# Performance work log

Measured on AMD Instinct MI355X. Metric: run time of the kernel, lower is better.

The kernel has to match this reference:

```python
import jax, jax.numpy as jnp
import numpy as np
from jax import lax

PATCH = 11          # patch_size
DIL = 2             # dilation_patch
PAD = (PATCH // 2) * DIL  # 10
EPS = 1e-5


def setup_inputs() -> dict:
    key = jax.random.key(0)
    k0, k1, kw, kb, kg, kbe = jax.random.split(key, 6)
    B, C, H, W = 8, 128, 192, 192
    x0 = jax.random.normal(k0, (B, C, H, W), dtype=jnp.float32)
    x1 = jax.random.normal(k1, (B, C, H, W), dtype=jnp.float32)
    # Conv2d(121, 8, k=3, s=1, p=1) params + BatchNorm2d(8) affine params
    conv_w = jax.random.normal(kw, (8, 121, 3, 3), dtype=jnp.float32) * 0.05
    conv_b = jax.random.normal(kb, (8,), dtype=jnp.float32) * 0.05
    gamma = jnp.ones((8,), dtype=jnp.float32)
    beta = jnp.zeros((8,), dtype=jnp.float32)
    return {"x0": x0, "x1": x1, "conv_w": conv_w, "conv_b": conv_b,
            "gamma": gamma, "beta": beta}


def _correlation(x0, x1):
    """spatial_correlation_sample(kernel=1, patch=11, stride=1, pad=0, dil_patch=2).
    out[b, pi*11+pj, i, j] = sum_c x0[b,c,i,j] * x1[b,c, i+(pi-5)*2, j+(pj-5)*2]
    (zero-padded outside)."""
    x1p = jnp.pad(x1, ((0, 0), (0, 0), (PAD, PAD), (PAD, PAD)))
    slices = []
    for pi in range(PATCH):       # static 11x11 displacement grid
        for pj in range(PATCH):
            x1s = lax.dynamic_slice(x1p, (0, 0, pi * DIL, pj * DIL), x1.shape)
            slices.append(jnp.einsum('bchw,bchw->bhw', x0, x1s))
    return jnp.stack(slices, axis=1)  # [B, 121, H, W]


def reference(x0, x1, conv_w, conv_b, gamma, beta):
    y = _correlation(x0, x1)  # [B, 121, H, W]
    y = lax.conv_general_dilated(y, conv_w, window_strides=(1, 1),
                                 padding=((1, 1), (1, 1)),
                                 dimension_numbers=('NCHW', 'OIHW', 'NCHW'))
    y = y + conv_b[None, :, None, None]
    # BatchNorm2d in training mode: batch statistics over (B, H, W), biased var
    mean = jnp.mean(y, axis=(0, 2, 3))
    var = jnp.var(y, axis=(0, 2, 3))
    y = (y - mean[None, :, None, None]) * (gamma / jnp.sqrt(var + EPS))[None, :, None, None] \
        + beta[None, :, None, None]
    return jax.nn.relu(y)
```

## Files before the change

kernel.cpp:

```cpp
#include <hip/hip_runtime.h>

#define HH 192
#define WW 192
#define CC 128
#define BB 8
#define HW (HH * WW)
#define OC 8
#define NPIX (BB * HW)
#define YCHUNK (OC * BB * HW)
#define X0ROW 24576
#define X1ROW 28672

typedef __attribute__((ext_vector_type(8))) short bf16x8;
typedef __attribute__((ext_vector_type(4))) float f32x4;

__device__ __forceinline__ unsigned short f2bf(float f) {
    unsigned int u = __float_as_uint(f);
    u += 0x7fffu + ((u >> 16) & 1u);
    return (unsigned short)(u >> 16);
}

__global__ __launch_bounds__(256) void k_pack(
    const float* __restrict__ x0, const float* __restrict__ x1,
    unsigned short* __restrict__ x0t, unsigned short* __restrict__ x1t)
{
    const int h = blockIdx.x, b = blockIdx.y, t = blockIdx.z;
    const float* src = t ? x1 : x0;
    __shared__ unsigned short lds[WW * 130];

    for (int idx = threadIdx.x; idx < CC * WW; idx += 256) {
        const int w = idx % WW, c = idx / WW;
        lds[w * 130 + c] = f2bf(src[((size_t)(b * CC + c) * HH + h) * WW + w]);
    }
    __syncthreads();

    if (t == 0) {
        unsigned int* dst = (unsigned int*)(x0t + (size_t)(b * HH + h) * X0ROW);
        for (int f2 = threadIdx.x; f2 < X0ROW / 2; f2 += 256) {
            const int e2  = f2 & 3;
            const int pxl = (f2 >> 2) & 15;
            const int kg  = (f2 >> 6) & 3;
            const int q   = (f2 >> 8) & 3;
            const int pu  = f2 >> 10;
            const int ut  = pu % 6, par = pu / 6;
            const int px  = 2 * (16 * ut + pxl) + par;
            const int c   = q * 32 + kg * 8 + e2 * 2;
            const unsigned int lo = lds[px * 130 + c];
            const unsigned int hi = lds[px * 130 + c + 1];
            dst[f2] = lo | (hi << 16);
        }
    } else {
        unsigned int* dst = (unsigned int*)(x1t + (size_t)(b * HH + h) * X1ROW);
        for (int f2 = threadIdx.x; f2 < X1ROW / 2; f2 += 256) {
            const int e2  = f2 & 3;
            const int pxl = (f2 >> 2) & 15;
            const int kg  = (f2 >> 6) & 3;
            const int q   = (f2 >> 8) & 3;
            const int pv  = f2 >> 10;
            const int vt  = pv % 7, par = pv / 7;
            const int v   = 16 * vt - 8 + pxl;
            unsigned int val = 0;
            if (v >= 0 && v < 96) {
                const int px = 2 * v + par;
                const int c  = q * 32 + kg * 8 + e2 * 2;
                val = lds[px * 130 + c] | ((unsigned int)lds[px * 130 + c + 1] << 16);
            }
            dst[f2] = val;
        }
    }
}

__global__ __launch_bounds__(384, 3) void k_corr_mfma_conv(
    const unsigned short* __restrict__ x0t, const unsigned short* __restrict__ x1t,
    const float* __restrict__ cw, const float* __restrict__ cb,
    float* __restrict__ y0, float* __restrict__ y1)
{
    const int L = blockIdx.x;
    const int w = (L & 7) * 64 + (L >> 3);
    const int b     = w >> 6;
    const int rem   = w & 63;
    const int part  = rem >> 5;
    const int strip = rem & 31;
    const int i0    = strip * 6;
    const int plo   = part ? 6 : 0;
    const int phi   = part ? 11 : 6;

    const int tid  = threadIdx.x;
    const int wave = tid >> 6, lane = tid & 63;
    const int ln15 = lane & 15, kg = lane >> 4;
    const int u0   = wave * 16;

    __shared__ float corr[8][194][11];

    if (tid < 176) {
        const int ir = tid / 22, rr = tid % 22;
        const int pj = rr % 11, jj = (rr < 11) ? 0 : 193;
        corr[ir][jj][pj] = 0.f;
    }

    float yacc[3][OC];
#pragma unroll
    for (int k = 0; k < 3; ++k)
#pragma unroll
        for (int o = 0; o < OC; ++o) yacc[k][o] = 0.f;

    const int jt  = tid % 192;
    const int irb = tid / 192;

    const unsigned short* x0b = x0t + (size_t)b * HH * X0ROW;
    const unsigned short* x1b = x1t + (size_t)b * HH * X1ROW;

    for (int pi = plo; pi < phi; ++pi) {
        __syncthreads();

        for (int ir = 0; ir < 8; ++ir) {
            const int i = i0 - 1 + ir;
            const int r = i + 2 * pi - 10;
            const bool gv = (i >= 0) && (i < HH) && (r >= 0) && (r < HH);
            const int icl = min(max(i, 0), HH - 1);
            const int rcl = min(max(r, 0), HH - 1);
            const unsigned short* arow = x0b + (size_t)icl * X0ROW + lane * 8;
            const unsigned short* brow = x1b + (size_t)rcl * X1ROW + lane * 8;

#pragma unroll
            for (int par = 0; par < 2; ++par) {
                const unsigned short* pa = arow + (par * 6 + wave) * 2048;
                const bf16x8 a0 = *(const bf16x8*)(pa);
                const bf16x8 a1 = *(const bf16x8*)(pa + 512);
                const bf16x8 a2 = *(const bf16x8*)(pa + 1024);
                const bf16x8 a3 = *(const bf16x8*)(pa + 1536);

#pragma unroll
                for (int vtl = 0; vtl < 2; ++vtl) {
                    const unsigned short* pb =
                        brow + (par * 7 + wave + vtl) * 2048;
                    const bf16x8 b0 = *(const bf16x8*)(pb);
                    const bf16x8 b1 = *(const bf16x8*)(pb + 512);
                    const bf16x8 b2 = *(const bf16x8*)(pb + 1024);
                    const bf16x8 b3 = *(const bf16x8*)(pb + 1536);

                    f32x4 c = {0.f, 0.f, 0.f, 0.f};
                    c = __builtin_amdgcn_mfma_f32_16x16x32_bf16(a0, b0, c, 0, 0, 0);
                    c = __builtin_amdgcn_mfma_f32_16x16x32_bf16(a1, b1, c, 0, 0, 0);
                    c = __builtin_amdgcn_mfma_f32_16x16x32_bf16(a2, b2, c, 0, 0, 0);
                    c = __builtin_amdgcn_mfma_f32_16x16x32_bf16(a3, b3, c, 0, 0, 0);

                    const int v = u0 - 8 + 16 * vtl + ln15;
#pragma unroll
                    for (int rg = 0; rg < 4; ++rg) {
                        const int u  = u0 + kg * 4 + rg;
                        const int pj = v - u + 5;
                        if (pj >= 0 && pj < 11)
                            corr[ir][2 * u + par + 1][pj] = gv ? c[rg] : 0.f;
                    }
                }
            }
        }
        __syncthreads();

        for (int ki = 0; ki < 3; ++ki) {
            for (int kj = 0; kj < 3; ++kj) {
                float cv[3][11];
#pragma unroll
                for (int k = 0; k < 3; ++k) {
                    const float* cp = &corr[irb + 2 * k + ki][jt + kj][0];
#pragma unroll
                    for (int pj = 0; pj < 11; ++pj) cv[k][pj] = cp[pj];
                }
#pragma unroll
                for (int o = 0; o < OC; ++o) {
                    float a0 = yacc[0][o], a1 = yacc[1][o], a2 = yacc[2][o];
#pragma unroll
                    for (int pj = 0; pj < 11; ++pj) {
                        const float wv =
                            cw[o * 1089 + (pi * 11 + pj) * 9 + ki * 3 + kj];
                        a0 = fmaf(wv, cv[0][pj], a0);
                        a1 = fmaf(wv, cv[1][pj], a1);
                        a2 = fmaf(wv, cv[2][pj], a2);
                    }
                    yacc[0][o] = a0; yacc[1][o] = a1; yacc[2][o] = a2;
                }
            }
        }
    }

    float* yp = part ? y1 : y0;
#pragma unroll
    for (int k = 0; k < 3; ++k) {
        const int irow = i0 + irb + 2 * k;
#pragma unroll
        for (int o = 0; o < OC; ++o) {
            float val = yacc[k][o];
            if (part == 0) val += cb[o];
            yp[((size_t)(b * OC + o) * HH + irow) * WW + jt] = val;
        }
    }
}

__global__ __launch_bounds__(256) void k_corr_conv(
    const float* __restrict__ x0, const float* __restrict__ x1,
    const float* __restrict__ cw, const float* __restrict__ cb,
    float* __restrict__ y)
{
    const int b  = blockIdx.z;
    const int i0 = blockIdx.y * 14;
    const int j0 = blockIdx.x * 14;
    const int li = threadIdx.x >> 4;
    const int lj = threadIdx.x & 15;
    const int gi = i0 + li - 1;
    const int gj = j0 + lj - 1;
    const bool valid    = (gi >= 0) & (gi < HH) & (gj >= 0) & (gj < WW);
    const bool interior = (li >= 1) & (li <= 14) & (lj >= 1) & (lj <= 14)
                        & (gi < HH) & (gj < WW);

    __shared__ float corr[16][16][13];

    float yacc[OC];
#pragma unroll
    for (int o = 0; o < OC; ++o) yacc[o] = 0.f;

    const size_t bbase = (size_t)b * CC * HW;
    const float* x0p = x0 + bbase + (size_t)gi * WW + gj;

    for (int pi = 0; pi < 11; ++pi) {
        float acc[11];
#pragma unroll
        for (int k = 0; k < 11; ++k) acc[k] = 0.f;

        const int r = gi + 2 * pi - 10;
        if (valid && r >= 0 && r < HH) {
            const float* p0 = x0p;
            if (gj >= 10 && gj <= WW - 11) {
                const float* p1o = x1 + bbase + (size_t)r * WW + (gj - 10);
#pragma unroll 2
                for (int c = 0; c < CC; ++c) {
                    const float a = *p0;
#pragma unroll
                    for (int k = 0; k < 11; ++k)
                        acc[k] = fmaf(a, p1o[2 * k], acc[k]);
                    p0 += HW; p1o += HW;
                }
            } else {
                const float* p1 = x1 + bbase + (size_t)r * WW;
#pragma unroll 2
                for (int c = 0; c < CC; ++c) {
                    const float a = *p0;
#pragma unroll
                    for (int k = 0; k < 11; ++k) {
                        const int col = gj + 2 * k - 10;
                        const float v = (col >= 0 && col < WW) ? p1[col] : 0.f;
                        acc[k] = fmaf(a, v, acc[k]);
                    }
                    p0 += HW; p1 += HW;
                }
            }
        }

        __syncthreads();
#pragma unroll
        for (int k = 0; k < 11; ++k) corr[li][lj][k] = acc[k];
        __syncthreads();

        if (interior) {
#pragma unroll
            for (int ki = 0; ki < 3; ++ki) {
#pragma unroll
                for (int kj = 0; kj < 3; ++kj) {
                    float cv[11];
#pragma unroll
                    for (int k = 0; k < 11; ++k)
                        cv[k] = corr[li + ki - 1][lj + kj - 1][k];
#pragma unroll
                    for (int o = 0; o < OC; ++o) {
#pragma unroll
                        for (int k = 0; k < 11; ++k) {
                            const float wv =
                                cw[(((o * 121) + pi * 11 + k) * 3 + ki) * 3 + kj];
                            yacc[o] = fmaf(wv, cv[k], yacc[o]);
                        }
                    }
                }
            }
        }
    }

    if (interior) {
#pragma unroll
        for (int o = 0; o < OC; ++o)
            y[(size_t)(b * OC + o) * HW + (size_t)gi * WW + gj] = yacc[o] + cb[o];
    }
}

__global__ __launch_bounds__(256) void k_stats_partial(
    const float* __restrict__ y0, const float* __restrict__ y1, int add2,
    float* __restrict__ st)
{
    const int bid = blockIdx.x;
    const int b = bid >> 5, rem = bid & 31;
    const int o = rem >> 2, q = rem & 3;
    const size_t off = (size_t)(b * OC + o) * (HW / 4) + q * (HW / 16);
    const float4* p0 = (const float4*)y0 + off;
    const float4* p1 = (const float4*)y1 + off;
    float s = 0.f, qq = 0.f;
    for (int t = threadIdx.x; t < HW / 16; t += 256) {
        float4 z = p0[t];
        if (add2) {
            const float4 v = p1[t];
            z.x += v.x; z.y += v.y; z.z += v.z; z.w += v.w;
        }
        s += z.x + z.y + z.z + z.w;
        qq = fmaf(z.x, z.x, qq); qq = fmaf(z.y, z.y, qq);
        qq = fmaf(z.z, z.z, qq); qq = fmaf(z.w, z.w, qq);
    }
#pragma unroll
    for (int off2 = 32; off2 > 0; off2 >>= 1) {
        s  += __shfl_down(s, off2);
        qq += __shfl_down(qq, off2);
    }
    __shared__ float ss[4], sq[4];
    const int lane = threadIdx.x & 63, wv = threadIdx.x >> 6;
    if (lane == 0) { ss[wv] = s; sq[wv] = qq; }
    __syncthreads();
    if (threadIdx.x == 0) {
        st[bid]       = ss[0] + ss[1] + ss[2] + ss[3];
        st[256 + bid] = sq[0] + sq[1] + sq[2] + sq[3];
    }
}

__global__ void k_stats_final(float* __restrict__ st,
                              const float* __restrict__ gamma,
                              const float* __restrict__ beta)
{
    const int o = threadIdx.x;
    if (o < 8) {
        float S = 0.f, Q = 0.f;
#pragma unroll
        for (int b = 0; b < 8; ++b)
#pragma unroll
            for (int q = 0; q < 4; ++q) {
                S += st[b * 32 + o * 4 + q];
                Q += st[256 + b * 32 + o * 4 + q];
            }
        const float invN = 1.f / (float)NPIX;
        const float mean = S * invN;
        const float var  = Q * invN - mean * mean;
        const float sc   = gamma[o] / sqrtf(var + 1e-5f);
        st[512 + o] = sc;
        st[520 + o] = beta[o] - mean * sc;
    }
}

__global__ __launch_bounds__(256) void k_bn_relu(
    const float* __restrict__ y0, const float* __restrict__ y1, int add2,
    const float* __restrict__ st, float* __restrict__ out)
{
    const int i = blockIdx.x * 256 + threadIdx.x;
    const int o = (i / (HW / 4)) & 7;
    const float sc = st[512 + o], sh = st[520 + o];
    float4 z = ((const float4*)y0)[i];
    if (add2) {
        const float4 v = ((const float4*)y1)[i];
        z.x += v.x; z.y += v.y; z.z += v.z; z.w += v.w;
    }
    float4 r;
    r.x = fmaxf(fmaf(z.x, sc, sh), 0.f);
    r.y = fmaxf(fmaf(z.y, sc, sh), 0.f);
    r.z = fmaxf(fmaf(z.z, sc, sh), 0.f);
    r.w = fmaxf(fmaf(z.w, sc, sh), 0.f);
    ((float4*)out)[i] = r;
}

extern "C" void kernel_launch(void* const* d_in, const int* in_sizes, int n_in,
                              void* d_out, int out_size, void* d_ws, size_t ws_size,
                              hipStream_t stream)
{
    const float* x0    = (const float*)d_in[0];
    const float* x1    = (const float*)d_in[1];
    const float* cw    = (const float*)d_in[2];
    const float* cb    = (const float*)d_in[3];
    const float* gamma = (const float*)d_in[4];
    const float* beta  = (const float*)d_in[5];
    float* out = (float*)d_out;
    float* st  = (float*)d_ws;

    const size_t x0bytes = (size_t)BB * HH * X0ROW * sizeof(unsigned short);
    const size_t x1bytes = (size_t)BB * HH * X1ROW * sizeof(unsigned short);
    const size_t ybytes  = (size_t)YCHUNK * sizeof(float);

    if (ws_size >= x0bytes + x1bytes + ybytes) {
        unsigned short* x0t = (unsigned short*)d_ws;
        unsigned short* x1t = (unsigned short*)((char*)d_ws + x0bytes);
        float* y1           = (float*)((char*)d_ws + x0bytes + x1bytes);

        k_pack<<<dim3(HH, BB, 2), 256, 0, stream>>>(x0, x1, x0t, x1t);
        k_corr_mfma_conv<<<512, 384, 0, stream>>>(x0t, x1t, cw, cb, out, y1);
        k_stats_partial<<<256, 256, 0, stream>>>(out, y1, 1, st);
        k_stats_final<<<1, 64, 0, stream>>>(st, gamma, beta);
        k_bn_relu<<<(YCHUNK / 4) / 256, 256, 0, stream>>>(out, y1, 1, st, out);
    } else {
        dim3 g1(14, 14, 8);
        k_corr_conv<<<g1, 256, 0, stream>>>(x0, x1, cw, cb, out);
        k_stats_partial<<<256, 256, 0, stream>>>(out, out, 0, st);
        k_stats_final<<<1, 64, 0, stream>>>(st, gamma, beta);
        k_bn_relu<<<(YCHUNK / 4) / 256, 256, 0, stream>>>(out, out, 0, st, out);
    }
}
```

Before: 561.1 us.

## Split correlation rows three ways and store LDS correlation tile as bf16

The fused correlation+conv kernel now splits the 11 displacement rows across three blocks per strip instead of two, launching 768 blocks and writing a third partial output buffer that the stats and BN kernels sum. The shared correlation tile is stored as bf16 instead of fp32, halving LDS per block, and the launch bounds now request 8 blocks per CU instead of 3. This aims for higher occupancy and more parallelism. The cost is extra workspace, more partial-sum traffic, and lost precision in the intermediate correlation values before the conv.

```diff
diff --git a/kernel.cpp b/kernel.cpp
--- a/kernel.cpp
+++ b/kernel.cpp
@@ -18,6 +18,9 @@
     unsigned int u = __float_as_uint(f);
     u += 0x7fffu + ((u >> 16) & 1u);
     return (unsigned short)(u >> 16);
+}
+__device__ __forceinline__ float bf2f(unsigned short u) {
+    return __uint_as_float(((unsigned int)u) << 16);
 }
 
 __global__ __launch_bounds__(256) void k_pack(
@@ -70,32 +73,32 @@
     }
 }
 
-__global__ __launch_bounds__(384, 3) void k_corr_mfma_conv(
+__global__ __launch_bounds__(384, 8) void k_corr_mfma_conv(
     const unsigned short* __restrict__ x0t, const unsigned short* __restrict__ x1t,
     const float* __restrict__ cw, const float* __restrict__ cb,
-    float* __restrict__ y0, float* __restrict__ y1)
+    float* __restrict__ y0, float* __restrict__ y1, float* __restrict__ y2)
 {
     const int L = blockIdx.x;
-    const int w = (L & 7) * 64 + (L >> 3);
-    const int b     = w >> 6;
-    const int rem   = w & 63;
+    const int w = (L & 7) * 96 + (L >> 3);
+    const int b     = w / 96;
+    const int rem   = w % 96;
     const int part  = rem >> 5;
     const int strip = rem & 31;
     const int i0    = strip * 6;
-    const int plo   = part ? 6 : 0;
-    const int phi   = part ? 11 : 6;
+    const int plo   = (11 * part) / 3;
+    const int phi   = (11 * (part + 1)) / 3;
 
     const int tid  = threadIdx.x;
     const int wave = tid >> 6, lane = tid & 63;
     const int ln15 = lane & 15, kg = lane >> 4;
     const int u0   = wave * 16;
 
-    __shared__ float corr[8][194][11];
+    __shared__ unsigned short corr[8][194][11];
 
     if (tid < 176) {
         const int ir = tid / 22, rr = tid % 22;
         const int pj = rr % 11, jj = (rr < 11) ? 0 : 193;
-        corr[ir][jj][pj] = 0.f;
+        corr[ir][jj][pj] = 0;
     }
 
     float yacc[3][OC];
@@ -151,7 +154,7 @@
                         const int u  = u0 + kg * 4 + rg;
                         const int pj = v - u + 5;
                         if (pj >= 0 && pj < 11)
-                            corr[ir][2 * u + par + 1][pj] = gv ? c[rg] : 0.f;
+                            corr[ir][2 * u + par + 1][pj] = f2bf(gv ? c[rg] : 0.f);
                     }
                 }
             }
@@ -163,9 +166,9 @@
                 float cv[3][11];
 #pragma unroll
                 for (int k = 0; k < 3; ++k) {
-                    const float* cp = &corr[irb + 2 * k + ki][jt + kj][0];
-#pragma unroll
-                    for (int pj = 0; pj < 11; ++pj) cv[k][pj] = cp[pj];
+                    const unsigned short* cp = &corr[irb + 2 * k + ki][jt + kj][0];
+#pragma unroll
+                    for (int pj = 0; pj < 11; ++pj) cv[k][pj] = bf2f(cp[pj]);
                 }
 #pragma unroll
                 for (int o = 0; o < OC; ++o) {
@@ -184,7 +187,7 @@
         }
     }
 
-    float* yp = part ? y1 : y0;
+    float* yp = (part == 0) ? y0 : ((part == 1) ? y1 : y2);
 #pragma unroll
     for (int k = 0; k < 3; ++k) {
         const int irow = i0 + irb + 2 * k;
@@ -292,8 +295,8 @@
 }
 
 __global__ __launch_bounds__(256) void k_stats_partial(
-    const float* __restrict__ y0, const float* __restrict__ y1, int add2,
-    float* __restrict__ st)
+    const float* __restrict__ y0, const float* __restrict__ y1,
+    const float* __restrict__ y2, int n, float* __restrict__ st)
 {
     const int bid = blockIdx.x;
     const int b = bid >> 5, rem = bid & 31;
@@ -301,11 +304,16 @@
     const size_t off = (size_t)(b * OC + o) * (HW / 4) + q * (HW / 16);
     const float4* p0 = (const float4*)y0 + off;
     const float4* p1 = (const float4*)y1 + off;
+    const float4* p2 = (const float4*)y2 + off;
     float s = 0.f, qq = 0.f;
     for (int t = threadIdx.x; t < HW / 16; t += 256) {
         float4 z = p0[t];
-        if (add2) {
+        if (n >= 2) {
             const float4 v = p1[t];
+            z.x += v.x; z.y += v.y; z.z += v.z; z.w += v.w;
+        }
+        if (n >= 3) {
+            const float4 v = p2[t];
             z.x += v.x; z.y += v.y; z.z += v.z; z.w += v.w;
         }
         s += z.x + z.y + z.z + z.w;
@@ -351,15 +359,20 @@
 }
 
 __global__ __launch_bounds__(256) void k_bn_relu(
-    const float* __restrict__ y0, const float* __restrict__ y1, int add2,
+    const float* __restrict__ y0, const float* __restrict__ y1,
+    const float* __restrict__ y2, int n,
     const float* __restrict__ st, float* __restrict__ out)
 {
     const int i = blockIdx.x * 256 + threadIdx.x;
     const int o = (i / (HW / 4)) & 7;
     const float sc = st[512 + o], sh = st[520 + o];
     float4 z = ((const float4*)y0)[i];
-    if (add2) {
+    if (n >= 2) {
         const float4 v = ((const float4*)y1)[i];
+        z.x += v.x; z.y += v.y; z.z += v.z; z.w += v.w;
+    }
+    if (n >= 3) {
+        const float4 v = ((const float4*)y2)[i];
         z.x += v.x; z.y += v.y; z.z += v.z; z.w += v.w;
     }
     float4 r;
@@ -387,21 +400,22 @@
     const size_t x1bytes = (size_t)BB * HH * X1ROW * sizeof(unsigned short);
     const size_t ybytes  = (size_t)YCHUNK * sizeof(float);
 
-    if (ws_size >= x0bytes + x1bytes + ybytes) {
+    if (ws_size >= x0bytes + x1bytes + 2 * ybytes) {
         unsigned short* x0t = (unsigned short*)d_ws;
         unsigned short* x1t = (unsigned short*)((char*)d_ws + x0bytes);
         float* y1           = (float*)((char*)d_ws + x0bytes + x1bytes);
+        float* y2           = (float*)((char*)d_ws + x0bytes + x1bytes + ybytes);
 
         k_pack<<<dim3(HH, BB, 2), 256, 0, stream>>>(x0, x1, x0t, x1t);
-        k_corr_mfma_conv<<<512, 384, 0, stream>>>(x0t, x1t, cw, cb, out, y1);
-        k_stats_partial<<<256, 256, 0, stream>>>(out, y1, 1, st);
+        k_corr_mfma_conv<<<768, 384, 0, stream>>>(x0t, x1t, cw, cb, out, y1, y2);
+        k_stats_partial<<<256, 256, 0, stream>>>(out, y1, y2, 3, st);
         k_stats_final<<<1, 64, 0, stream>>>(st, gamma, beta);
-        k_bn_relu<<<(YCHUNK / 4) / 256, 256, 0, stream>>>(out, y1, 1, st, out);
+        k_bn_relu<<<(YCHUNK / 4) / 256, 256, 0, stream>>>(out, y1, y2, 3, st, out);
     } else {
         dim3 g1(14, 14, 8);
         k_corr_conv<<<g1, 256, 0, stream>>>(x0, x1, cw, cb, out);
-        k_stats_partial<<<256, 256, 0, stream>>>(out, out, 0, st);
+        k_stats_partial<<<256, 256, 0, stream>>>(out, out, out, 1, st);
         k_stats_final<<<1, 64, 0, stream>>>(st, gamma, beta);
-        k_bn_relu<<<(YCHUNK / 4) / 256, 256, 0, stream>>>(out, out, 0, st, out);
-    }
-}
+        k_bn_relu<<<(YCHUNK / 4) / 256, 256, 0, stream>>>(out, out, out, 1, st, out);
+    }
+}
```

Result: faster. 530.9 us (-5.4%).

## Double-buffer x1 rows in LDS, split parity across 12 waves, store corr as bf16

Applied to the files above, without the earlier changes.

The fused correlation+conv kernel now runs 768 threads, with each wave handling one parity/u-tile instead of looping over parity. Each x1 row is staged into a double-buffered LDS area, and the next row's x1 data and x0 A-fragments are prefetched into registers while the current row's MFMAs run. The correlation scratch is stored as bf16 to cut LDS use, which lowers the precision of the intermediate. The conv phase uses only 576 of the 768 threads, leaving the rest idle there. The pack kernel now writes 16-byte vectors, and the workspace check asks for extra space.

```diff
diff --git a/kernel.cpp b/kernel.cpp
--- a/kernel.cpp
+++ b/kernel.cpp
@@ -19,6 +19,9 @@
     u += 0x7fffu + ((u >> 16) & 1u);
     return (unsigned short)(u >> 16);
 }
+__device__ __forceinline__ float bf2f(unsigned short u) {
+    return __uint_as_float(((unsigned int)u) << 16);
+}
 
 __global__ __launch_bounds__(256) void k_pack(
     const float* __restrict__ x0, const float* __restrict__ x1,
@@ -35,42 +38,46 @@
     __syncthreads();
 
     if (t == 0) {
-        unsigned int* dst = (unsigned int*)(x0t + (size_t)(b * HH + h) * X0ROW);
-        for (int f2 = threadIdx.x; f2 < X0ROW / 2; f2 += 256) {
-            const int e2  = f2 & 3;
-            const int pxl = (f2 >> 2) & 15;
-            const int kg  = (f2 >> 6) & 3;
-            const int q   = (f2 >> 8) & 3;
-            const int pu  = f2 >> 10;
+        uint4* dst = (uint4*)(x0t + (size_t)(b * HH + h) * X0ROW);
+        for (int f8 = threadIdx.x; f8 < X0ROW / 8; f8 += 256) {
+            const int pxl = f8 & 15;
+            const int kg  = (f8 >> 4) & 3;
+            const int q   = (f8 >> 6) & 3;
+            const int pu  = f8 >> 8;
             const int ut  = pu % 6, par = pu / 6;
             const int px  = 2 * (16 * ut + pxl) + par;
-            const int c   = q * 32 + kg * 8 + e2 * 2;
-            const unsigned int lo = lds[px * 130 + c];
-            const unsigned int hi = lds[px * 130 + c + 1];
-            dst[f2] = lo | (hi << 16);
+            const unsigned short* s0 = &lds[px * 130 + q * 32 + kg * 8];
+            uint4 v;
+            v.x = s0[0] | ((unsigned int)s0[1] << 16);
+            v.y = s0[2] | ((unsigned int)s0[3] << 16);
+            v.z = s0[4] | ((unsigned int)s0[5] << 16);
+            v.w = s0[6] | ((unsigned int)s0[7] << 16);
+            dst[f8] = v;
         }
     } else {
-        unsigned int* dst = (unsigned int*)(x1t + (size_t)(b * HH + h) * X1ROW);
-        for (int f2 = threadIdx.x; f2 < X1ROW / 2; f2 += 256) {
-            const int e2  = f2 & 3;
-            const int pxl = (f2 >> 2) & 15;
-            const int kg  = (f2 >> 6) & 3;
-            const int q   = (f2 >> 8) & 3;
-            const int pv  = f2 >> 10;
+        uint4* dst = (uint4*)(x1t + (size_t)(b * HH + h) * X1ROW);
+        for (int f8 = threadIdx.x; f8 < X1ROW / 8; f8 += 256) {
+            const int pxl = f8 & 15;
+            const int kg  = (f8 >> 4) & 3;
+            const int q   = (f8 >> 6) & 3;
+            const int pv  = f8 >> 8;
             const int vt  = pv % 7, par = pv / 7;
             const int v   = 16 * vt - 8 + pxl;
-            unsigned int val = 0;
+            uint4 val = {0u, 0u, 0u, 0u};
             if (v >= 0 && v < 96) {
                 const int px = 2 * v + par;
-                const int c  = q * 32 + kg * 8 + e2 * 2;
-                val = lds[px * 130 + c] | ((unsigned int)lds[px * 130 + c + 1] << 16);
-            }
-            dst[f2] = val;
-        }
-    }
-}
-
-__global__ __launch_bounds__(384, 3) void k_corr_mfma_conv(
+                const unsigned short* s0 = &lds[px * 130 + q * 32 + kg * 8];
+                val.x = s0[0] | ((unsigned int)s0[1] << 16);
+                val.y = s0[2] | ((unsigned int)s0[3] << 16);
+                val.z = s0[4] | ((unsigned int)s0[5] << 16);
+                val.w = s0[6] | ((unsigned int)s0[7] << 16);
+            }
+            dst[f8] = val;
+        }
+    }
+}
+
+__global__ __launch_bounds__(768, 3) void k_corr_mfma_conv(
     const unsigned short* __restrict__ x0t, const unsigned short* __restrict__ x1t,
     const float* __restrict__ cw, const float* __restrict__ cb,
     float* __restrict__ y0, float* __restrict__ y1)
@@ -88,62 +95,101 @@
     const int tid  = threadIdx.x;
     const int wave = tid >> 6, lane = tid & 63;
     const int ln15 = lane & 15, kg = lane >> 4;
-    const int u0   = wave * 16;
-
-    __shared__ float corr[8][194][11];
+    const int par  = wave / 6, ut = wave % 6;
+    const int u0   = ut * 16;
+
+    __shared__ unsigned short corr[8][194][11];
+    __shared__ uint4 Bbuf[2][3840];
 
     if (tid < 176) {
         const int ir = tid / 22, rr = tid % 22;
         const int pj = rr % 11, jj = (rr < 11) ? 0 : 193;
-        corr[ir][jj][pj] = 0.f;
-    }
-
-    float yacc[3][OC];
-#pragma unroll
-    for (int k = 0; k < 3; ++k)
+        corr[ir][jj][pj] = 0;
+    }
+
+    const int quad = tid / 192;
+    const int jt   = tid % 192;
+
+    float yacc[2][OC];
+#pragma unroll
+    for (int k = 0; k < 2; ++k)
 #pragma unroll
         for (int o = 0; o < OC; ++o) yacc[k][o] = 0.f;
-
-    const int jt  = tid % 192;
-    const int irb = tid / 192;
 
     const unsigned short* x0b = x0t + (size_t)b * HH * X0ROW;
     const unsigned short* x1b = x1t + (size_t)b * HH * X1ROW;
 
+    const int soff0 = tid * 16;
+
+    bf16x8 A[2][4];
+
     for (int pi = plo; pi < phi; ++pi) {
-        __syncthreads();
-
+        {
+            const int r0  = min(max(i0 - 1 + 2 * pi - 10, 0), HH - 1);
+            const char* rsrc = (const char*)(x1b + (size_t)r0 * X1ROW);
+            uint4 R[5];
+#pragma unroll
+            for (int s = 0; s < 5; ++s) {
+                const int off = soff0 + s * 12288;
+                if (off < 57344) R[s] = *(const uint4*)(rsrc + off);
+            }
+            const int icl = min(max(i0 - 1, 0), HH - 1);
+            const unsigned short* pa =
+                x0b + (size_t)icl * X0ROW + wave * 2048 + lane * 8;
+            A[0][0] = *(const bf16x8*)(pa);
+            A[0][1] = *(const bf16x8*)(pa + 512);
+            A[0][2] = *(const bf16x8*)(pa + 1024);
+            A[0][3] = *(const bf16x8*)(pa + 1536);
+
+            __syncthreads();
+#pragma unroll
+            for (int s = 0; s < 5; ++s) {
+                const int off = soff0 + s * 12288;
+                if (off < 57344) *(uint4*)((char*)&Bbuf[0][0] + off) = R[s];
+            }
+            __syncthreads();
+        }
+
+#pragma unroll
         for (int ir = 0; ir < 8; ++ir) {
-            const int i = i0 - 1 + ir;
-            const int r = i + 2 * pi - 10;
-            const bool gv = (i >= 0) && (i < HH) && (r >= 0) && (r < HH);
-            const int icl = min(max(i, 0), HH - 1);
-            const int rcl = min(max(r, 0), HH - 1);
-            const unsigned short* arow = x0b + (size_t)icl * X0ROW + lane * 8;
-            const unsigned short* brow = x1b + (size_t)rcl * X1ROW + lane * 8;
-
-#pragma unroll
-            for (int par = 0; par < 2; ++par) {
-                const unsigned short* pa = arow + (par * 6 + wave) * 2048;
-                const bf16x8 a0 = *(const bf16x8*)(pa);
-                const bf16x8 a1 = *(const bf16x8*)(pa + 512);
-                const bf16x8 a2 = *(const bf16x8*)(pa + 1024);
-                const bf16x8 a3 = *(const bf16x8*)(pa + 1536);
+            uint4 R[5];
+            if (ir < 7) {
+                const int rn = min(max(i0 + ir + 2 * pi - 10, 0), HH - 1);
+                const char* rsrc = (const char*)(x1b + (size_t)rn * X1ROW);
+#pragma unroll
+                for (int s = 0; s < 5; ++s) {
+                    const int off = soff0 + s * 12288;
+                    if (off < 57344) R[s] = *(const uint4*)(rsrc + off);
+                }
+                const int icl = min(max(i0 + ir, 0), HH - 1);
+                const unsigned short* pa =
+                    x0b + (size_t)icl * X0ROW + wave * 2048 + lane * 8;
+                A[(ir + 1) & 1][0] = *(const bf16x8*)(pa);
+                A[(ir + 1) & 1][1] = *(const bf16x8*)(pa + 512);
+                A[(ir + 1) & 1][2] = *(const bf16x8*)(pa + 1024);
+                A[(ir + 1) & 1][3] = *(const bf16x8*)(pa + 1536);
+            }
+
+            {
+                const int i = i0 - 1 + ir;
+                const int r = i + 2 * pi - 10;
+                const bool gv = (i >= 0) && (i < HH) && (r >= 0) && (r < HH);
+                const char* bb = (const char*)&Bbuf[ir & 1][0];
 
 #pragma unroll
                 for (int vtl = 0; vtl < 2; ++vtl) {
-                    const unsigned short* pb =
-                        brow + (par * 7 + wave + vtl) * 2048;
+                    const char* pb =
+                        bb + (par * 7 + ut + vtl) * 4096 + lane * 16;
                     const bf16x8 b0 = *(const bf16x8*)(pb);
-                    const bf16x8 b1 = *(const bf16x8*)(pb + 512);
-                    const bf16x8 b2 = *(const bf16x8*)(pb + 1024);
-                    const bf16x8 b3 = *(const bf16x8*)(pb + 1536);
+                    const bf16x8 b1 = *(const bf16x8*)(pb + 1024);
+                    const bf16x8 b2 = *(const bf16x8*)(pb + 2048);
+                    const bf16x8 b3 = *(const bf16x8*)(pb + 3072);
 
                     f32x4 c = {0.f, 0.f, 0.f, 0.f};
-                    c = __builtin_amdgcn_mfma_f32_16x16x32_bf16(a0, b0, c, 0, 0, 0);
-                    c = __builtin_amdgcn_mfma_f32_16x16x32_bf16(a1, b1, c, 0, 0, 0);
-                    c = __builtin_amdgcn_mfma_f32_16x16x32_bf16(a2, b2, c, 0, 0, 0);
-                    c = __builtin_amdgcn_mfma_f32_16x16x32_bf16(a3, b3, c, 0, 0, 0);
+                    c = __builtin_amdgcn_mfma_f32_16x16x32_bf16(A[ir & 1][0], b0, c, 0, 0, 0);
+                    c = __builtin_amdgcn_mfma_f32_16x16x32_bf16(A[ir & 1][1], b1, c, 0, 0, 0);
+                    c = __builtin_amdgcn_mfma_f32_16x16x32_bf16(A[ir & 1][2], b2, c, 0, 0, 0);
+                    c = __builtin_amdgcn_mfma_f32_16x16x32_bf16(A[ir & 1][3], b3, c, 0, 0, 0);
 
                     const int v = u0 - 8 + 16 * vtl + ln15;
 #pragma unroll
@@ -151,48 +197,62 @@
                         const int u  = u0 + kg * 4 + rg;
                         const int pj = v - u + 5;
                         if (pj >= 0 && pj < 11)
-                            corr[ir][2 * u + par + 1][pj] = gv ? c[rg] : 0.f;
+                            corr[ir][2 * u + par + 1][pj] = f2bf(gv ? c[rg] : 0.f);
                     }
                 }
             }
-        }
-        __syncthreads();
-
-        for (int ki = 0; ki < 3; ++ki) {
-            for (int kj = 0; kj < 3; ++kj) {
-                float cv[3][11];
-#pragma unroll
-                for (int k = 0; k < 3; ++k) {
-                    const float* cp = &corr[irb + 2 * k + ki][jt + kj][0];
-#pragma unroll
-                    for (int pj = 0; pj < 11; ++pj) cv[k][pj] = cp[pj];
-                }
-#pragma unroll
-                for (int o = 0; o < OC; ++o) {
-                    float a0 = yacc[0][o], a1 = yacc[1][o], a2 = yacc[2][o];
-#pragma unroll
-                    for (int pj = 0; pj < 11; ++pj) {
-                        const float wv =
-                            cw[o * 1089 + (pi * 11 + pj) * 9 + ki * 3 + kj];
-                        a0 = fmaf(wv, cv[0][pj], a0);
-                        a1 = fmaf(wv, cv[1][pj], a1);
-                        a2 = fmaf(wv, cv[2][pj], a2);
+            __syncthreads();
+
+            if (ir < 7) {
+#pragma unroll
+                for (int s = 0; s < 5; ++s) {
+                    const int off = soff0 + s * 12288;
+                    if (off < 57344)
+                        *(uint4*)((char*)&Bbuf[(ir + 1) & 1][0] + off) = R[s];
+                }
+                __syncthreads();
+            }
+        }
+
+        if (quad < 3) {
+            for (int ki = 0; ki < 3; ++ki) {
+                for (int kj = 0; kj < 3; ++kj) {
+                    float cv[2][11];
+#pragma unroll
+                    for (int k = 0; k < 2; ++k) {
+                        const unsigned short* cp =
+                            &corr[quad * 2 + k + ki][jt + kj][0];
+#pragma unroll
+                        for (int pj = 0; pj < 11; ++pj) cv[k][pj] = bf2f(cp[pj]);
                     }
-                    yacc[0][o] = a0; yacc[1][o] = a1; yacc[2][o] = a2;
-                }
-            }
-        }
-    }
-
-    float* yp = part ? y1 : y0;
-#pragma unroll
-    for (int k = 0; k < 3; ++k) {
-        const int irow = i0 + irb + 2 * k;
-#pragma unroll
-        for (int o = 0; o < OC; ++o) {
-            float val = yacc[k][o];
-            if (part == 0) val += cb[o];
-            yp[((size_t)(b * OC + o) * HH + irow) * WW + jt] = val;
+#pragma unroll
+                    for (int o = 0; o < OC; ++o) {
+                        float a0 = yacc[0][o], a1 = yacc[1][o];
+#pragma unroll
+                        for (int pj = 0; pj < 11; ++pj) {
+                            const float wv =
+                                cw[o * 1089 + (pi * 11 + pj) * 9 + ki * 3 + kj];
+                            a0 = fmaf(wv, cv[0][pj], a0);
+                            a1 = fmaf(wv, cv[1][pj], a1);
+                        }
+                        yacc[0][o] = a0; yacc[1][o] = a1;
+                    }
+                }
+            }
+        }
+    }
+
+    if (quad < 3) {
+        float* yp = part ? y1 : y0;
+#pragma unroll
+        for (int k = 0; k < 2; ++k) {
+            const int irow = i0 + quad * 2 + k;
+#pragma unroll
+            for (int o = 0; o < OC; ++o) {
+                float val = yacc[k][o];
+                if (part == 0) val += cb[o];
+                yp[((size_t)(b * OC + o) * HH + irow) * WW + jt] = val;
+            }
         }
     }
 }
@@ -387,13 +447,13 @@
     const size_t x1bytes = (size_t)BB * HH * X1ROW * sizeof(unsigned short);
     const size_t ybytes  = (size_t)YCHUNK * sizeof(float);
 
-    if (ws_size >= x0bytes + x1bytes + ybytes) {
+    if (ws_size >= x0bytes + x1bytes + ybytes + 65536) {
         unsigned short* x0t = (unsigned short*)d_ws;
         unsigned short* x1t = (unsigned short*)((char*)d_ws + x0bytes);
         float* y1           = (float*)((char*)d_ws + x0bytes + x1bytes);
 
         k_pack<<<dim3(HH, BB, 2), 256, 0, stream>>>(x0, x1, x0t, x1t);
-        k_corr_mfma_conv<<<512, 384, 0, stream>>>(x0t, x1t, cw, cb, out, y1);
+        k_corr_mfma_conv<<<512, 768, 0, stream>>>(x0t, x1t, cw, cb, out, y1);
         k_stats_partial<<<256, 256, 0, stream>>>(out, y1, 1, st);
         k_stats_final<<<1, 64, 0, stream>>>(st, gamma, beta);
         k_bn_relu<<<(YCHUNK / 4) / 256, 256, 0, stream>>>(out, y1, 1, st, out);
```

Result: slower. 1.009 ms (+79.9%).
